# Optimization experiments

Measured on AMD Instinct MI355X. Metric: run time of the kernel, lower is better.

## Reference

```python
import jax, jax.numpy as jnp
import numpy as np

MEAN = 0.0
STD = 0.04
STEP = 2

def setup_inputs() -> dict:
    key = jax.random.key(0)
    k1, k2 = jax.random.split(key)
    B, L = 512, 100000
    x = jax.random.normal(k1, (B, L), dtype=jnp.float32)
    noise = jax.random.normal(k2, (L,), dtype=jnp.float32)
    move = 100  # deterministic stand-in for RandomLoopMove's random shift
    return {"x": x, "noise": noise, "move": move}

def reference(x, noise, move):
    B, L = x.shape
    # LoopMove: circular shift along the trace axis
    x = jnp.roll(x, move, axis=1)
    # AddGaussianNoise: single noise vector (randn*std + mean) added to every row
    x = x + (noise * STD + MEAN)
    # Integrate(step=2, mode='mean'): segment-mean over non-overlapping windows,
    # each pooled value written to positions 2j and 2j+1 (exactly fills the trace)
    pooled = jnp.mean(x.reshape(B, L // STEP, STEP), axis=2)  # [B, L/2]
    x = jnp.repeat(pooled, STEP, axis=1)                      # [B, L]
    # Normalize: per-row standardization (np.std uses ddof=0)
    mu = jnp.mean(x, axis=1, keepdims=True)
    sd = jnp.std(x, axis=1, keepdims=True)
    return (x - mu) / sd
```

## Files before the change

### kernel.cpp

```cpp
#include <hip/hip_runtime.h>


#define THREADS 1024
#define NWAVES (THREADS / 64)
#define KMAX 25

__global__ __launch_bounds__(THREADS) void tbt_kernel(
    const float* __restrict__ x,
    const float* __restrict__ noise,
    const int* __restrict__ movep,
    float* __restrict__ out,
    int L)
{
    const int b   = blockIdx.x;
    const int tid = threadIdx.x;
    const int J   = L >> 1;

    int mv = movep[0];
    mv %= L;
    if (mv < 0) mv += L;

    const float* __restrict__ xrow = x + (size_t)b * (size_t)L;
    float* __restrict__ orow       = out + (size_t)b * (size_t)L;

    const bool fast4 = ((mv & 3) == 0) && ((L & 3) == 0);
    const bool fast2 = ((mv & 1) == 0) && ((L & 1) == 0);

    const int U  = J >> 1;
    const int nk = (U + THREADS - 1) / THREADS;

    float sum = 0.f, sumsq = 0.f;

    if (fast4 && nk <= KMAX) {
        float p[2 * KMAX];

        #pragma unroll
        for (int k = 0; k < KMAX; ++k) {
            const int u = tid + k * THREADS;
            if (u < U) {
                int s = 4 * u - mv; if (s < 0) s += L;
                float4 v = *(const float4*)(xrow + s);
                float4 n = *(const float4*)(noise + 4 * u);
                float a = 0.5f * (v.x + v.y) + 0.02f * (n.x + n.y);
                float c = 0.5f * (v.z + v.w) + 0.02f * (n.z + n.w);
                p[2 * k]     = a;
                p[2 * k + 1] = c;
                sum   += a + c;
                sumsq += a * a + c * c;
            }
        }

        #pragma unroll
        for (int off = 32; off > 0; off >>= 1) {
            sum   += __shfl_down(sum,   off, 64);
            sumsq += __shfl_down(sumsq, off, 64);
        }

        __shared__ float s_sum[NWAVES], s_sq[NWAVES];
        __shared__ float s_mu, s_isd;
        const int wave = tid >> 6;
        const int lane = tid & 63;
        if (lane == 0) { s_sum[wave] = sum; s_sq[wave] = sumsq; }
        __syncthreads();
        if (tid == 0) {
            float ts = 0.f, tq = 0.f;
            #pragma unroll
            for (int w = 0; w < NWAVES; ++w) { ts += s_sum[w]; tq += s_sq[w]; }
            float invJ = 1.0f / (float)J;
            float mu   = ts * invJ;
            float var  = tq * invJ - mu * mu;
            s_mu  = mu;
            s_isd = rsqrtf(fmaxf(var, 1e-30f));
        }
        __syncthreads();
        const float mu  = s_mu;
        const float isd = s_isd;

        #pragma unroll
        for (int k = 0; k < KMAX; ++k) {
            const int u = tid + k * THREADS;
            if (u < U) {
                float r0 = (p[2 * k]     - mu) * isd;
                float r1 = (p[2 * k + 1] - mu) * isd;
                *(float4*)(orow + 4 * u) = make_float4(r0, r0, r1, r1);
            }
        }
        return;
    }

    for (int j = tid; j < J; j += THREADS) {
        int s = 2 * j - mv;
        if (s < 0) s += L;
        float a, c;
        if (fast2) {
            float2 v = *(const float2*)(xrow + s);
            a = v.x; c = v.y;
        } else {
            int s1 = s + 1; if (s1 >= L) s1 -= L;
            a = xrow[s]; c = xrow[s1];
        }
        float2 nv = *(const float2*)(noise + 2 * j);
        float p = 0.5f * (a + c + 0.04f * (nv.x + nv.y));
        sum   += p;
        sumsq += p * p;
    }

    #pragma unroll
    for (int off = 32; off > 0; off >>= 1) {
        sum   += __shfl_down(sum,   off, 64);
        sumsq += __shfl_down(sumsq, off, 64);
    }

    __shared__ float f_sum[NWAVES], f_sq[NWAVES];
    __shared__ float f_mu, f_isd;
    const int wave = tid >> 6;
    const int lane = tid & 63;
    if (lane == 0) { f_sum[wave] = sum; f_sq[wave] = sumsq; }
    __syncthreads();
    if (tid == 0) {
        float ts = 0.f, tq = 0.f;
        #pragma unroll
        for (int w = 0; w < NWAVES; ++w) { ts += f_sum[w]; tq += f_sq[w]; }
        float invJ = 1.0f / (float)J;
        float mu   = ts * invJ;
        float var  = tq * invJ - mu * mu;
        f_mu  = mu;
        f_isd = rsqrtf(fmaxf(var, 1e-30f));
    }
    __syncthreads();
    const float mu  = f_mu;
    const float isd = f_isd;

    for (int j = tid; j < J; j += THREADS) {
        int s = 2 * j - mv;
        if (s < 0) s += L;
        float a, c;
        if (fast2) {
            float2 v = *(const float2*)(xrow + s);
            a = v.x; c = v.y;
        } else {
            int s1 = s + 1; if (s1 >= L) s1 -= L;
            a = xrow[s]; c = xrow[s1];
        }
        float2 nv = *(const float2*)(noise + 2 * j);
        float p = 0.5f * (a + c + 0.04f * (nv.x + nv.y));
        float r = (p - mu) * isd;
        *(float2*)(orow + 2 * j) = make_float2(r, r);
    }
}

extern "C" void kernel_launch(void* const* d_in, const int* in_sizes, int n_in,
                              void* d_out, int out_size, void* d_ws, size_t ws_size,
                              hipStream_t stream) {
    const float* x     = (const float*)d_in[0];
    const float* noise = (const float*)d_in[1];
    const int*   move  = (const int*)d_in[2];
    float*       out   = (float*)d_out;

    const int L = in_sizes[1];
    const int B = in_sizes[0] / L;

    tbt_kernel<<<B, THREADS, 0, stream>>>(x, noise, move, out, L);
}
```

Baseline: 349.0 us.

## Split per-row normalization into two slice-parallel passes with a workspace reduction

The single 1024-thread-per-row kernel, which held the pooled row in registers, is replaced by two kernels over B×4 blocks of 256 threads. Pass 1 writes partial sum and sum-of-squares per slice to the workspace. Pass 2 combines the partials, recomputes the pooled values from x and writes with nontemporal stores. This aims to raise occupancy and memory-level parallelism, at the cost of reading x twice, which may partly come from the large last-level cache. The split path does not check that the shift is a multiple of 4, unlike the old fast path, so it is only correct for such shifts.

```diff
diff --git a/kernel.cpp b/kernel.cpp
--- a/kernel.cpp
+++ b/kernel.cpp
@@ -1,4 +1,108 @@
 #include <hip/hip_runtime.h>
+
+
+#define SLICES 4
+#define K_THREADS 256
+
+typedef float f32x4 __attribute__((ext_vector_type(4)));
+
+__global__ __launch_bounds__(K_THREADS) void tbt_pass1(
+    const float* __restrict__ x,
+    const float* __restrict__ noise,
+    const int* __restrict__ movep,
+    float* __restrict__ ws,
+    int L)
+{
+    const int bid = blockIdx.x;
+    const int row = bid / SLICES;
+    const int sl  = bid % SLICES;
+    const int tid = threadIdx.x;
+    const int J   = L >> 1;
+    const int U   = J >> 1;
+    const int U4  = U / SLICES;
+    const int u0  = sl * U4;
+    const int u1  = u0 + U4;
+
+    int mv = movep[0];
+    mv %= L; if (mv < 0) mv += L;
+
+    const float* __restrict__ xrow = x + (size_t)row * (size_t)L;
+
+    float sum = 0.f, sq = 0.f;
+    #pragma unroll 2
+    for (int u = u0 + tid; u < u1; u += K_THREADS) {
+        int s = 4 * u - mv; if (s < 0) s += L;
+        float4 v = *(const float4*)(xrow + s);
+        float4 n = *(const float4*)(noise + 4 * u);
+        float a = 0.5f * (v.x + v.y) + 0.02f * (n.x + n.y);
+        float c = 0.5f * (v.z + v.w) + 0.02f * (n.z + n.w);
+        sum += a + c;
+        sq  += a * a + c * c;
+    }
+
+    #pragma unroll
+    for (int off = 32; off > 0; off >>= 1) {
+        sum += __shfl_down(sum, off, 64);
+        sq  += __shfl_down(sq,  off, 64);
+    }
+
+    __shared__ float s_sum[K_THREADS / 64], s_sq[K_THREADS / 64];
+    const int wave = tid >> 6;
+    if ((tid & 63) == 0) { s_sum[wave] = sum; s_sq[wave] = sq; }
+    __syncthreads();
+    if (tid == 0) {
+        float ts = 0.f, tq = 0.f;
+        #pragma unroll
+        for (int w = 0; w < K_THREADS / 64; ++w) { ts += s_sum[w]; tq += s_sq[w]; }
+        ws[2 * bid]     = ts;
+        ws[2 * bid + 1] = tq;
+    }
+}
+
+__global__ __launch_bounds__(K_THREADS) void tbt_pass2(
+    const float* __restrict__ x,
+    const float* __restrict__ noise,
+    const int* __restrict__ movep,
+    const float* __restrict__ ws,
+    float* __restrict__ out,
+    int L)
+{
+    const int bid = blockIdx.x;
+    const int row = bid / SLICES;
+    const int sl  = bid % SLICES;
+    const int tid = threadIdx.x;
+    const int J   = L >> 1;
+    const int U   = J >> 1;
+    const int U4  = U / SLICES;
+    const int u0  = sl * U4;
+    const int u1  = u0 + U4;
+
+    int mv = movep[0];
+    mv %= L; if (mv < 0) mv += L;
+
+    const float* wr = ws + (size_t)row * 2 * SLICES;
+    float ts = 0.f, tq = 0.f;
+    #pragma unroll
+    for (int i = 0; i < SLICES; ++i) { ts += wr[2 * i]; tq += wr[2 * i + 1]; }
+    const float invJ = 1.0f / (float)J;
+    const float mu   = ts * invJ;
+    const float var  = tq * invJ - mu * mu;
+    const float isd  = rsqrtf(fmaxf(var, 1e-30f));
+
+    const float* __restrict__ xrow = x + (size_t)row * (size_t)L;
+    float* __restrict__ orow       = out + (size_t)row * (size_t)L;
+
+    #pragma unroll 2
+    for (int u = u0 + tid; u < u1; u += K_THREADS) {
+        int s = 4 * u - mv; if (s < 0) s += L;
+        float4 v = *(const float4*)(xrow + s);
+        float4 n = *(const float4*)(noise + 4 * u);
+        float r0 = (0.5f * (v.x + v.y) + 0.02f * (n.x + n.y) - mu) * isd;
+        float r1 = (0.5f * (v.z + v.w) + 0.02f * (n.z + n.w) - mu) * isd;
+        f32x4 o = {r0, r0, r1, r1};
+        __builtin_nontemporal_store(o, (f32x4*)(orow + 4 * u));
+    }
+}
 
 
 #define THREADS 1024
@@ -17,8 +121,7 @@
     const int J   = L >> 1;
 
     int mv = movep[0];
-    mv %= L;
-    if (mv < 0) mv += L;
+    mv %= L; if (mv < 0) mv += L;
 
     const float* __restrict__ xrow = x + (size_t)b * (size_t)L;
     float* __restrict__ orow       = out + (size_t)b * (size_t)L;
@@ -160,5 +263,18 @@
     const int L = in_sizes[1];
     const int B = in_sizes[0] / L;
 
-    tbt_kernel<<<B, THREADS, 0, stream>>>(x, noise, move, out, L);
-}
+    const int J = L >> 1;
+    const int U = J >> 1;
+    const size_t ws_need = (size_t)B * SLICES * 2 * sizeof(float);
+
+    const bool split_ok = ((L & 3) == 0) && (U % SLICES == 0) &&
+                          (ws_size >= ws_need) && (d_ws != nullptr);
+
+    if (split_ok) {
+        float* ws = (float*)d_ws;
+        tbt_pass1<<<B * SLICES, K_THREADS, 0, stream>>>(x, noise, move, ws, L);
+        tbt_pass2<<<B * SLICES, K_THREADS, 0, stream>>>(x, noise, move, ws, out, L);
+    } else {
+        tbt_kernel<<<B, THREADS, 0, stream>>>(x, noise, move, out, L);
+    }
+}
```

New measurement: 377.5 us. +8.2%, slower.

## Process two rows per block, overlapping second row loads with first row stores

Applied to the files above, without the earlier changes.

Adds a kernel where each block handles two rows: while the second row is being loaded and reduced, the normalized output of the first row is written, so reads and writes overlap inside one block. Global loads and stores of x and out switch to nontemporal builtins to avoid polluting cache. This halves the grid to 256 blocks and doubles the per-thread register buffer, which can lower occupancy and leave CUs underused on a large GPU.

```diff
diff --git a/kernel.cpp b/kernel.cpp
--- a/kernel.cpp
+++ b/kernel.cpp
@@ -4,6 +4,155 @@
 #define THREADS 1024
 #define NWAVES (THREADS / 64)
 #define KMAX 25
+
+typedef float f32x4 __attribute__((ext_vector_type(4)));
+
+__device__ __forceinline__ void row_stats(
+    float sum, float sq, int tid, int J,
+    float* s_sum, float* s_sq, float* s_mu, float* s_isd,
+    float& mu, float& isd)
+{
+    #pragma unroll
+    for (int off = 32; off > 0; off >>= 1) {
+        sum += __shfl_down(sum, off, 64);
+        sq  += __shfl_down(sq,  off, 64);
+    }
+    const int wave = tid >> 6;
+    if ((tid & 63) == 0) { s_sum[wave] = sum; s_sq[wave] = sq; }
+    __syncthreads();
+    if (tid == 0) {
+        float ts = 0.f, tq = 0.f;
+        #pragma unroll
+        for (int w = 0; w < NWAVES; ++w) { ts += s_sum[w]; tq += s_sq[w]; }
+        float invJ = 1.0f / (float)J;
+        float m   = ts * invJ;
+        float var = tq * invJ - m * m;
+        *s_mu  = m;
+        *s_isd = rsqrtf(fmaxf(var, 1e-30f));
+    }
+    __syncthreads();
+    mu  = *s_mu;
+    isd = *s_isd;
+}
+
+__device__ __forceinline__ void generic_row(
+    const float* __restrict__ xrow, const float* __restrict__ noise,
+    float* __restrict__ orow, int L, int mv, int tid,
+    float* s_sum, float* s_sq, float* s_mu, float* s_isd)
+{
+    const int J = L >> 1;
+    const bool fast2 = ((mv & 1) == 0) && ((L & 1) == 0);
+    float sum = 0.f, sq = 0.f;
+    for (int j = tid; j < J; j += THREADS) {
+        int s = 2 * j - mv; if (s < 0) s += L;
+        float a, c;
+        if (fast2) { float2 v = *(const float2*)(xrow + s); a = v.x; c = v.y; }
+        else { int s1 = s + 1; if (s1 >= L) s1 -= L; a = xrow[s]; c = xrow[s1]; }
+        float2 nv = *(const float2*)(noise + 2 * j);
+        float p = 0.5f * (a + c + 0.04f * (nv.x + nv.y));
+        sum += p; sq += p * p;
+    }
+    float mu, isd;
+    row_stats(sum, sq, tid, J, s_sum, s_sq, s_mu, s_isd, mu, isd);
+    for (int j = tid; j < J; j += THREADS) {
+        int s = 2 * j - mv; if (s < 0) s += L;
+        float a, c;
+        if (fast2) { float2 v = *(const float2*)(xrow + s); a = v.x; c = v.y; }
+        else { int s1 = s + 1; if (s1 >= L) s1 -= L; a = xrow[s]; c = xrow[s1]; }
+        float2 nv = *(const float2*)(noise + 2 * j);
+        float p = 0.5f * (a + c + 0.04f * (nv.x + nv.y));
+        float r = (p - mu) * isd;
+        *(float2*)(orow + 2 * j) = make_float2(r, r);
+    }
+}
+
+__global__ __launch_bounds__(THREADS) void tbt_pipe(
+    const float* __restrict__ x,
+    const float* __restrict__ noise,
+    const int* __restrict__ movep,
+    float* __restrict__ out,
+    int L)
+{
+    const int tid = threadIdx.x;
+    const int J = L >> 1;
+    const int U = J >> 1;
+
+    int mv = movep[0];
+    mv %= L; if (mv < 0) mv += L;
+
+    const size_t roff = (size_t)(2 * blockIdx.x) * (size_t)L;
+    const float* __restrict__ xr0 = x + roff;
+    const float* __restrict__ xr1 = xr0 + L;
+    float* __restrict__ or0 = out + roff;
+    float* __restrict__ or1 = or0 + L;
+
+    __shared__ float s_sum[NWAVES], s_sq[NWAVES];
+    __shared__ float s_stat[4];
+
+    const bool fast4 = ((mv & 3) == 0) && ((L & 3) == 0);
+    if (!fast4) {
+        generic_row(xr0, noise, or0, L, mv, tid, s_sum, s_sq, &s_stat[0], &s_stat[1]);
+        __syncthreads();
+        generic_row(xr1, noise, or1, L, mv, tid, s_sum, s_sq, &s_stat[2], &s_stat[3]);
+        return;
+    }
+
+    float p0[2 * KMAX], p1[2 * KMAX];
+    float sum = 0.f, sq = 0.f;
+
+    #pragma unroll
+    for (int k = 0; k < KMAX; ++k) {
+        const int u = tid + k * THREADS;
+        if (u < U) {
+            int s = 4 * u - mv; if (s < 0) s += L;
+            f32x4 v = __builtin_nontemporal_load((const f32x4*)(xr0 + s));
+            float4 n = *(const float4*)(noise + 4 * u);
+            float a = 0.5f * (v.x + v.y) + 0.02f * (n.x + n.y);
+            float c = 0.5f * (v.z + v.w) + 0.02f * (n.z + n.w);
+            p0[2 * k]     = a;
+            p0[2 * k + 1] = c;
+            sum += a + c;
+            sq  += a * a + c * c;
+        }
+    }
+    float mu0, isd0;
+    row_stats(sum, sq, tid, J, s_sum, s_sq, &s_stat[0], &s_stat[1], mu0, isd0);
+
+    sum = 0.f; sq = 0.f;
+    #pragma unroll
+    for (int k = 0; k < KMAX; ++k) {
+        const int u = tid + k * THREADS;
+        if (u < U) {
+            int s = 4 * u - mv; if (s < 0) s += L;
+            f32x4 v = __builtin_nontemporal_load((const f32x4*)(xr1 + s));
+            float4 n = *(const float4*)(noise + 4 * u);
+            float ra = (p0[2 * k]     - mu0) * isd0;
+            float rc = (p0[2 * k + 1] - mu0) * isd0;
+            f32x4 o = {ra, ra, rc, rc};
+            __builtin_nontemporal_store(o, (f32x4*)(or0 + 4 * u));
+            float a = 0.5f * (v.x + v.y) + 0.02f * (n.x + n.y);
+            float c = 0.5f * (v.z + v.w) + 0.02f * (n.z + n.w);
+            p1[2 * k]     = a;
+            p1[2 * k + 1] = c;
+            sum += a + c;
+            sq  += a * a + c * c;
+        }
+    }
+    float mu1, isd1;
+    row_stats(sum, sq, tid, J, s_sum, s_sq, &s_stat[2], &s_stat[3], mu1, isd1);
+
+    #pragma unroll
+    for (int k = 0; k < KMAX; ++k) {
+        const int u = tid + k * THREADS;
+        if (u < U) {
+            float ra = (p1[2 * k]     - mu1) * isd1;
+            float rc = (p1[2 * k + 1] - mu1) * isd1;
+            f32x4 o = {ra, ra, rc, rc};
+            __builtin_nontemporal_store(o, (f32x4*)(or1 + 4 * u));
+        }
+    }
+}
+
 
 __global__ __launch_bounds__(THREADS) void tbt_kernel(
     const float* __restrict__ x,
@@ -17,136 +166,56 @@
     const int J   = L >> 1;
 
     int mv = movep[0];
-    mv %= L;
-    if (mv < 0) mv += L;
+    mv %= L; if (mv < 0) mv += L;
 
     const float* __restrict__ xrow = x + (size_t)b * (size_t)L;
     float* __restrict__ orow       = out + (size_t)b * (size_t)L;
 
     const bool fast4 = ((mv & 3) == 0) && ((L & 3) == 0);
-    const bool fast2 = ((mv & 1) == 0) && ((L & 1) == 0);
 
     const int U  = J >> 1;
     const int nk = (U + THREADS - 1) / THREADS;
 
-    float sum = 0.f, sumsq = 0.f;
+    __shared__ float s_sum[NWAVES], s_sq[NWAVES];
+    __shared__ float s_stat[2];
 
     if (fast4 && nk <= KMAX) {
         float p[2 * KMAX];
+        float sum = 0.f, sq = 0.f;
 
         #pragma unroll
         for (int k = 0; k < KMAX; ++k) {
             const int u = tid + k * THREADS;
             if (u < U) {
                 int s = 4 * u - mv; if (s < 0) s += L;
-                float4 v = *(const float4*)(xrow + s);
+                f32x4 v = __builtin_nontemporal_load((const f32x4*)(xrow + s));
                 float4 n = *(const float4*)(noise + 4 * u);
                 float a = 0.5f * (v.x + v.y) + 0.02f * (n.x + n.y);
                 float c = 0.5f * (v.z + v.w) + 0.02f * (n.z + n.w);
                 p[2 * k]     = a;
                 p[2 * k + 1] = c;
-                sum   += a + c;
-                sumsq += a * a + c * c;
+                sum += a + c;
+                sq  += a * a + c * c;
             }
         }
 
-        #pragma unroll
-        for (int off = 32; off > 0; off >>= 1) {
-            sum   += __shfl_down(sum,   off, 64);
-            sumsq += __shfl_down(sumsq, off, 64);
-        }
-
-        __shared__ float s_sum[NWAVES], s_sq[NWAVES];
-        __shared__ float s_mu, s_isd;
-        const int wave = tid >> 6;
-        const int lane = tid & 63;
-        if (lane == 0) { s_sum[wave] = sum; s_sq[wave] = sumsq; }
-        __syncthreads();
-        if (tid == 0) {
-            float ts = 0.f, tq = 0.f;
-            #pragma unroll
-            for (int w = 0; w < NWAVES; ++w) { ts += s_sum[w]; tq += s_sq[w]; }
-            float invJ = 1.0f / (float)J;
-            float mu   = ts * invJ;
-            float var  = tq * invJ - mu * mu;
-            s_mu  = mu;
-            s_isd = rsqrtf(fmaxf(var, 1e-30f));
-        }
-        __syncthreads();
-        const float mu  = s_mu;
-        const float isd = s_isd;
+        float mu, isd;
+        row_stats(sum, sq, tid, J, s_sum, s_sq, &s_stat[0], &s_stat[1], mu, isd);
 
         #pragma unroll
         for (int k = 0; k < KMAX; ++k) {
             const int u = tid + k * THREADS;
             if (u < U) {
-                float r0 = (p[2 * k]     - mu) * isd;
-                float r1 = (p[2 * k + 1] - mu) * isd;
-                *(float4*)(orow + 4 * u) = make_float4(r0, r0, r1, r1);
+                float ra = (p[2 * k]     - mu) * isd;
+                float rc = (p[2 * k + 1] - mu) * isd;
+                f32x4 o = {ra, ra, rc, rc};
+                __builtin_nontemporal_store(o, (f32x4*)(orow + 4 * u));
             }
         }
         return;
     }
 
-    for (int j = tid; j < J; j += THREADS) {
-        int s = 2 * j - mv;
-        if (s < 0) s += L;
-        float a, c;
-        if (fast2) {
-            float2 v = *(const float2*)(xrow + s);
-            a = v.x; c = v.y;
-        } else {
-            int s1 = s + 1; if (s1 >= L) s1 -= L;
-            a = xrow[s]; c = xrow[s1];
-        }
-        float2 nv = *(const float2*)(noise + 2 * j);
-        float p = 0.5f * (a + c + 0.04f * (nv.x + nv.y));
-        sum   += p;
-        sumsq += p * p;
-    }
-
-    #pragma unroll
-    for (int off = 32; off > 0; off >>= 1) {
-        sum   += __shfl_down(sum,   off, 64);
-        sumsq += __shfl_down(sumsq, off, 64);
-    }
-
-    __shared__ float f_sum[NWAVES], f_sq[NWAVES];
-    __shared__ float f_mu, f_isd;
-    const int wave = tid >> 6;
-    const int lane = tid & 63;
-    if (lane == 0) { f_sum[wave] = sum; f_sq[wave] = sumsq; }
-    __syncthreads();
-    if (tid == 0) {
-        float ts = 0.f, tq = 0.f;
-        #pragma unroll
-        for (int w = 0; w < NWAVES; ++w) { ts += f_sum[w]; tq += f_sq[w]; }
-        float invJ = 1.0f / (float)J;
-        float mu   = ts * invJ;
-        float var  = tq * invJ - mu * mu;
-        f_mu  = mu;
-        f_isd = rsqrtf(fmaxf(var, 1e-30f));
-    }
-    __syncthreads();
-    const float mu  = f_mu;
-    const float isd = f_isd;
-
-    for (int j = tid; j < J; j += THREADS) {
-        int s = 2 * j - mv;
-        if (s < 0) s += L;
-        float a, c;
-        if (fast2) {
-            float2 v = *(const float2*)(xrow + s);
-            a = v.x; c = v.y;
-        } else {
-            int s1 = s + 1; if (s1 >= L) s1 -= L;
-            a = xrow[s]; c = xrow[s1];
-        }
-        float2 nv = *(const float2*)(noise + 2 * j);
-        float p = 0.5f * (a + c + 0.04f * (nv.x + nv.y));
-        float r = (p - mu) * isd;
-        *(float2*)(orow + 2 * j) = make_float2(r, r);
-    }
+    generic_row(xrow, noise, orow, L, mv, tid, s_sum, s_sq, &s_stat[0], &s_stat[1]);
 }
 
 extern "C" void kernel_launch(void* const* d_in, const int* in_sizes, int n_in,
@@ -160,5 +229,13 @@
     const int L = in_sizes[1];
     const int B = in_sizes[0] / L;
 
-    tbt_kernel<<<B, THREADS, 0, stream>>>(x, noise, move, out, L);
-}
+    const int J  = L >> 1;
+    const int U  = J >> 1;
+    const int nk = (U + THREADS - 1) / THREADS;
+
+    if (((L & 3) == 0) && ((B & 1) == 0) && nk <= KMAX && B >= 2) {
+        tbt_pipe<<<B / 2, THREADS, 0, stream>>>(x, noise, move, out, L);
+    } else {
+        tbt_kernel<<<B, THREADS, 0, stream>>>(x, noise, move, out, L);
+    }
+}
```

Measured after the change: 336.5 us. 3.6% less time.
